# Performance work log

Hardware: AMD Instinct MI355X
Metric: run time of the kernel (lower is better)

Reference implementation:

```python
import jax, jax.numpy as jnp
import numpy as np

N_EMBD = 1024
N_HEAD = 16
HEAD_DIM = N_EMBD // N_HEAD


def setup_inputs() -> dict:
    key = jax.random.key(0)
    ks = jax.random.split(key, 9)
    B, T, C = 2, 2048, N_EMBD
    s = 1.0 / np.sqrt(C)
    inp = {
        "x": jax.random.normal(ks[0], (B, T, C), dtype=jnp.float32),
        "Wq": jax.random.normal(ks[1], (C, C), dtype=jnp.float32) * s,
        "bq": jnp.zeros((C,), dtype=jnp.float32),
        "Wk": jax.random.normal(ks[2], (C, C), dtype=jnp.float32) * s,
        "bk": jnp.zeros((C,), dtype=jnp.float32),
        "Wv": jax.random.normal(ks[3], (C, C), dtype=jnp.float32) * s,
        "bv": jnp.zeros((C,), dtype=jnp.float32),
        "Wo": jax.random.normal(ks[4], (C, C), dtype=jnp.float32) * s,
        "bo": jnp.zeros((C,), dtype=jnp.float32),
    }
    return inp


def reference(x, Wq, bq, Wk, bk, Wv, bv, Wo, bo):
    B, T, C = x.shape
    H, D = N_HEAD, HEAD_DIM
    # projections (torch Linear: x @ W^T + b)
    q = (x @ Wq.T + bq).reshape(B, T, H, D).transpose(0, 2, 1, 3)  # [B,H,T,D]
    k = (x @ Wk.T + bk).reshape(B, T, H, D).transpose(0, 2, 1, 3)
    v = (x @ Wv.T + bv).reshape(B, T, H, D).transpose(0, 2, 1, 3)
    scores = jnp.einsum("bhqd,bhkd->bhqk", q, k) / jnp.sqrt(jnp.asarray(D, x.dtype))
    causal = jnp.tril(jnp.ones((T, T), dtype=bool))
    scores = jnp.where(causal[None, None], scores, jnp.asarray(-jnp.inf, x.dtype))
    weights = jax.nn.softmax(scores, axis=-1)  # [B,H,T,T]
    attended = jnp.einsum("bhqk,bhkd->bhqd", weights, v)
    attended = attended.transpose(0, 2, 1, 3).reshape(B, T, C)
    return attended @ Wo.T + bo
```

## Files before the change

### kernel.cpp

```cpp
#include <hip/hip_runtime.h>

typedef unsigned short u16;
typedef __attribute__((ext_vector_type(8))) __bf16 bf16x8;
typedef __attribute__((ext_vector_type(4))) float f32x4;
typedef __attribute__((ext_vector_type(4))) unsigned int u32x4;

#define MFMA16(a, b, c) __builtin_amdgcn_mfma_f32_16x16x32_bf16(a, b, c, 0, 0, 0)

__device__ __forceinline__ u16 f2bf(float f) {
    unsigned u = __float_as_uint(f);
    u = (u + 0x7FFFu + ((u >> 16) & 1u)) >> 16;
    return (u16)u;
}

__device__ __forceinline__ void gl_lds16(const u16* g, u16* l) {
    __builtin_amdgcn_global_load_lds(
        (const __attribute__((address_space(1))) unsigned int*)g,
        (__attribute__((address_space(3))) unsigned int*)l, 16, 0, 0);
}

static constexpr int Bv = 2, Tv = 2048, Cv = 1024, Hv = 16, Dv = 64;
static constexpr int Mv = Bv * Tv;

static constexpr size_t OFF_XB = 0;
static constexpr size_t OFF_WQ = 4194304;
static constexpr size_t OFF_WK = OFF_WQ + 1048576;
static constexpr size_t OFF_WV = OFF_WK + 1048576;
static constexpr size_t OFF_WO = OFF_WV + 1048576;
static constexpr size_t OFF_Q  = OFF_WO + 1048576;
static constexpr size_t OFF_K  = OFF_Q + 4194304;
static constexpr size_t OFF_VT = OFF_K + 4194304;
static constexpr size_t OFF_A  = OFF_VT + 4194304;

__global__ __launch_bounds__(256) void convert_all(
    const float* __restrict__ x,
    const float* __restrict__ wq, const float* __restrict__ wk,
    const float* __restrict__ wv, const float* __restrict__ wo,
    u16* __restrict__ dst)
{
    int i4 = blockIdx.x * blockDim.x + threadIdx.x;
    if (i4 >= 2097152) return;
    int idx = i4 * 4;
    const float* src; int off;
    if (idx < 4194304) { src = x; off = idx; }
    else {
        int rel = idx - 4194304;
        int j = rel >> 20;
        off = rel & 1048575;
        src = (j == 0) ? wq : (j == 1) ? wk : (j == 2) ? wv : wo;
    }
    float4 v = *(const float4*)(src + off);
    ushort4 o;
    o.x = f2bf(v.x); o.y = f2bf(v.y); o.z = f2bf(v.z); o.w = f2bf(v.w);
    *(ushort4*)(dst + idx) = o;
}

template <bool OUT_BF16, bool ROWBIAS>
__device__ __forceinline__ void gemm128_b64(
    const u16* __restrict__ A, const u16* __restrict__ Wt,
    const float* __restrict__ bias, void* __restrict__ outp,
    int m0, int n0, int N, int K)
{
    __shared__ u16 lA[128 * 64];
    __shared__ u16 lB[128 * 64];
    const int tid  = threadIdx.x;
    const int lane = tid & 63, w = tid >> 6;
    const int quad = lane >> 4, lm = lane & 15;
    const int wm = (w & 1) * 64, wn = (w >> 1) * 64;

    f32x4 zero = {0.f, 0.f, 0.f, 0.f};
    f32x4 acc[4][4];
    #pragma unroll
    for (int mt = 0; mt < 4; mt++)
        #pragma unroll
        for (int nt = 0; nt < 4; nt++) acc[mt][nt] = zero;

    const int rowi = lane >> 3, seg = lane & 7;

    for (int k0 = 0; k0 < K; k0 += 64) {
        #pragma unroll
        for (int i = 0; i < 4; i++) {
            int rbase = w * 32 + i * 8;
            int row = rbase + rowi;
            int gseg = seg ^ (row & 7);
            gl_lds16(A  + (size_t)(m0 + row) * K + k0 + gseg * 8, &lA[rbase * 64]);
            gl_lds16(Wt + (size_t)(n0 + row) * K + k0 + gseg * 8, &lB[rbase * 64]);
        }
        __syncthreads();
        #pragma unroll
        for (int ks = 0; ks < 2; ks++) {
            const int swz = ((ks * 4 + quad) ^ (lm & 7)) * 8;
            bf16x8 af[4], bf[4];
            #pragma unroll
            for (int mt = 0; mt < 4; mt++)
                af[mt] = *(const bf16x8*)&lA[(wm + mt * 16 + lm) * 64 + swz];
            #pragma unroll
            for (int nt = 0; nt < 4; nt++)
                bf[nt] = *(const bf16x8*)&lB[(wn + nt * 16 + lm) * 64 + swz];
            #pragma unroll
            for (int mt = 0; mt < 4; mt++)
                #pragma unroll
                for (int nt = 0; nt < 4; nt++)
                    acc[mt][nt] = MFMA16(af[mt], bf[nt], acc[mt][nt]);
        }
        __syncthreads();
    }

    #pragma unroll
    for (int nt = 0; nt < 4; nt++) {
        int col = n0 + wn + nt * 16 + lm;
        float cb = ROWBIAS ? 0.f : bias[col];
        #pragma unroll
        for (int mt = 0; mt < 4; mt++) {
            #pragma unroll
            for (int r = 0; r < 4; r++) {
                int row = m0 + wm + mt * 16 + quad * 4 + r;
                float v = acc[mt][nt][r] + (ROWBIAS ? bias[row] : cb);
                if (OUT_BF16) ((u16*)outp)[(size_t)row * N + col] = f2bf(v);
                else          ((float*)outp)[(size_t)row * N + col] = v;
            }
        }
    }
}

__global__ __launch_bounds__(256) void gemm_qkv(
    const u16* __restrict__ A,
    const u16* __restrict__ Wq, const u16* __restrict__ Wk, const u16* __restrict__ Wv,
    const float* __restrict__ bq, const float* __restrict__ bk, const float* __restrict__ bv,
    u16* __restrict__ Q, u16* __restrict__ K, u16* __restrict__ VT)
{
    int nb = blockIdx.x;
    int which = nb >> 3;
    if (which == 0) {
        gemm128_b64<true, false>(A, Wq, bq, Q, blockIdx.y * 128, (nb & 7) * 128, Cv, Cv);
    } else if (which == 1) {
        gemm128_b64<true, false>(A, Wk, bk, K, blockIdx.y * 128, (nb & 7) * 128, Cv, Cv);
    } else {
        gemm128_b64<true, true>(Wv, A, bv, VT, (nb & 7) * 128, blockIdx.y * 128, Mv, Cv);
    }
}

__global__ __launch_bounds__(256) void gemm_o64(
    const u16* __restrict__ A, const u16* __restrict__ Wt,
    const float* __restrict__ bias, float* __restrict__ outp)
{
    __shared__ u16 lA[128 * 64];
    __shared__ u16 lB[64 * 64];
    const int tid  = threadIdx.x;
    const int lane = tid & 63, w = tid >> 6;
    const int quad = lane >> 4, lm = lane & 15;
    const int m0 = blockIdx.y * 128, n0 = blockIdx.x * 64;
    const int K = Cv;

    f32x4 zero = {0.f, 0.f, 0.f, 0.f};
    f32x4 acc[2][4];
    #pragma unroll
    for (int mt = 0; mt < 2; mt++)
        #pragma unroll
        for (int nt = 0; nt < 4; nt++) acc[mt][nt] = zero;

    const int rowi = lane >> 3, seg = lane & 7;

    for (int k0 = 0; k0 < K; k0 += 64) {
        #pragma unroll
        for (int i = 0; i < 4; i++) {
            int rbase = w * 32 + i * 8;
            int row = rbase + rowi;
            int gseg = seg ^ (row & 7);
            gl_lds16(A + (size_t)(m0 + row) * K + k0 + gseg * 8, &lA[rbase * 64]);
        }
        {
            int rbase = w * 16, row0 = rbase + rowi, row1 = row0 + 8;
            gl_lds16(Wt + (size_t)(n0 + row0) * K + k0 + (seg ^ (row0 & 7)) * 8, &lB[rbase * 64]);
            gl_lds16(Wt + (size_t)(n0 + row1) * K + k0 + (seg ^ (row1 & 7)) * 8, &lB[(rbase + 8) * 64]);
        }
        __syncthreads();
        #pragma unroll
        for (int ks = 0; ks < 2; ks++) {
            const int swz = ((ks * 4 + quad) ^ (lm & 7)) * 8;
            bf16x8 af[2], bf[4];
            #pragma unroll
            for (int mt = 0; mt < 2; mt++)
                af[mt] = *(const bf16x8*)&lA[(w * 32 + mt * 16 + lm) * 64 + swz];
            #pragma unroll
            for (int nt = 0; nt < 4; nt++)
                bf[nt] = *(const bf16x8*)&lB[(nt * 16 + lm) * 64 + swz];
            #pragma unroll
            for (int mt = 0; mt < 2; mt++)
                #pragma unroll
                for (int nt = 0; nt < 4; nt++)
                    acc[mt][nt] = MFMA16(af[mt], bf[nt], acc[mt][nt]);
        }
        __syncthreads();
    }

    #pragma unroll
    for (int nt = 0; nt < 4; nt++) {
        int col = n0 + nt * 16 + lm;
        float bvv = bias[col];
        #pragma unroll
        for (int mt = 0; mt < 2; mt++) {
            #pragma unroll
            for (int r = 0; r < 4; r++) {
                int row = m0 + w * 32 + mt * 16 + quad * 4 + r;
                outp[(size_t)row * Cv + col] = acc[mt][nt][r] + bvv;
            }
        }
    }
}

__global__ __launch_bounds__(512) void attn(
    const u16* __restrict__ Qp, const u16* __restrict__ Kp,
    const u16* __restrict__ VTg, u16* __restrict__ Op)
{
    __shared__ u16 lK[2][64 * 64];
    __shared__ u16 lVT[2][64 * 64];
    __shared__ u16 lP[8][32][72];

    const int tid  = threadIdx.x;
    const int lane = tid & 63, w = tid >> 6;
    const int g = w >> 2, wl = w & 3;
    const int quad = lane >> 4, lm = lane & 15;

    const int idx  = blockIdx.x;
    const int half = idx >> 8;
    const int grp  = idx & 255;
    const int bh   = (half << 4) | (grp >> 4);
    const int j    = grp & 15;
    const int qt   = half ? j : 15 - j;
    const int h = bh & 15, b = bh >> 4;

    const int qb = qt * 128;
    const size_t headoff = (size_t)b * Tv * Cv + (size_t)h * Dv;
    const size_t vthead  = (size_t)h * 64 * Mv + (size_t)b * Tv;

    bf16x8 qf[2][2];
    #pragma unroll
    for (int nt = 0; nt < 2; nt++) {
        const u16* qptr = Qp + headoff + (size_t)(qb + wl * 32 + nt * 16 + lm) * Cv + quad * 8;
        qf[0][nt] = *(const bf16x8*)(qptr);
        qf[1][nt] = *(const bf16x8*)(qptr + 32);
    }

    f32x4 zero = {0.f, 0.f, 0.f, 0.f};
    f32x4 oacc[2][4];
    #pragma unroll
    for (int mt = 0; mt < 2; mt++)
        #pragma unroll
        for (int nt = 0; nt < 4; nt++) oacc[mt][nt] = zero;
    float Lp[2] = {0.f, 0.f};

    const float SC = 0.18033688011112042f;
    const int rowi = lane >> 3, seg = lane & 7;

    auto stage = [&](int kt) {
        const int k0 = kt * 64;
        #pragma unroll
        for (int hf = 0; hf < 2; hf++) {
            int rbase = wl * 16 + hf * 8;
            int row = rbase + rowi;
            int gseg = seg ^ (row & 7);
            gl_lds16(Kp + headoff + (size_t)(k0 + row) * Cv + gseg * 8, &lK[g][rbase * 64]);
            gl_lds16(VTg + vthead + (size_t)row * Mv + k0 + gseg * 8, &lVT[g][rbase * 64]);
        }
    };

    auto body = [&](int kt, bool domask) __attribute__((always_inline)) {
        const int k0 = kt * 64;
        f32x4 stt[4][2];
        #pragma unroll
        for (int mt = 0; mt < 4; mt++)
            #pragma unroll
            for (int nt = 0; nt < 2; nt++) stt[mt][nt] = zero;
        #pragma unroll
        for (int ks = 0; ks < 2; ks++) {
            #pragma unroll
            for (int mt = 0; mt < 4; mt++) {
                bf16x8 kf = *(const bf16x8*)
                    &lK[g][(mt * 16 + lm) * 64 + (((ks * 4 + quad) ^ (lm & 7)) * 8)];
                #pragma unroll
                for (int nt = 0; nt < 2; nt++)
                    stt[mt][nt] = MFMA16(kf, qf[ks][nt], stt[mt][nt]);
            }
        }
        #pragma unroll
        for (int mt = 0; mt < 4; mt++) {
            #pragma unroll
            for (int nt = 0; nt < 2; nt++) {
                const int keyb = k0 + mt * 16 + quad * 4;
                const int qrow = qb + wl * 32 + nt * 16 + lm;
                float e0 = __builtin_amdgcn_exp2f(fmaf(stt[mt][nt][0], SC, -16.f));
                float e1 = __builtin_amdgcn_exp2f(fmaf(stt[mt][nt][1], SC, -16.f));
                float e2 = __builtin_amdgcn_exp2f(fmaf(stt[mt][nt][2], SC, -16.f));
                float e3 = __builtin_amdgcn_exp2f(fmaf(stt[mt][nt][3], SC, -16.f));
                if (domask) {
                    if (keyb + 0 > qrow) e0 = 0.f;
                    if (keyb + 1 > qrow) e1 = 0.f;
                    if (keyb + 2 > qrow) e2 = 0.f;
                    if (keyb + 3 > qrow) e3 = 0.f;
                }
                Lp[nt] += e0 + e1 + e2 + e3;
                ushort4 pk;
                pk.x = (u16)(__float_as_uint(e0) >> 16);
                pk.y = (u16)(__float_as_uint(e1) >> 16);
                pk.z = (u16)(__float_as_uint(e2) >> 16);
                pk.w = (u16)(__float_as_uint(e3) >> 16);
                *(ushort4*)&lP[w][nt * 16 + lm][mt * 16 + quad * 4] = pk;
            }
        }
        #pragma unroll
        for (int ks = 0; ks < 2; ks++) {
            bf16x8 pf[2];
            #pragma unroll
            for (int mt = 0; mt < 2; mt++)
                pf[mt] = *(const bf16x8*)&lP[w][mt * 16 + lm][ks * 32 + quad * 8];
            #pragma unroll
            for (int nt = 0; nt < 4; nt++) {
                bf16x8 vf = *(const bf16x8*)
                    &lVT[g][(nt * 16 + lm) * 64 + (((ks * 4 + quad) ^ (lm & 7)) * 8)];
                #pragma unroll
                for (int mt = 0; mt < 2; mt++)
                    oacc[mt][nt] = MFMA16(pf[mt], vf, oacc[mt][nt]);
            }
        }
    };

    for (int i = 0; i < qt; i++) {
        if (i) __syncthreads();
        stage(2 * i + g);
        __syncthreads();
        body(2 * i + g, false);
    }
    if (qt) __syncthreads();
    stage(2 * qt + g);
    __syncthreads();
    body(2 * qt + g, true);
    __syncthreads();

    float* lO = (float*)&lP[0][0][0];
    float* lL = lO + 32 * 256;
    const int t = tid & 255;
    if (g == 1) {
        #pragma unroll
        for (int mt = 0; mt < 2; mt++)
            #pragma unroll
            for (int nt = 0; nt < 4; nt++)
                #pragma unroll
                for (int r = 0; r < 4; r++)
                    lO[(mt * 16 + nt * 4 + r) * 256 + t] = oacc[mt][nt][r];
        lL[t] = Lp[0];
        lL[256 + t] = Lp[1];
    }
    __syncthreads();
    if (g == 0) {
        #pragma unroll
        for (int mt = 0; mt < 2; mt++)
            #pragma unroll
            for (int nt = 0; nt < 4; nt++)
                #pragma unroll
                for (int r = 0; r < 4; r++)
                    oacc[mt][nt][r] += lO[(mt * 16 + nt * 4 + r) * 256 + t];
        Lp[0] += lL[t];
        Lp[1] += lL[256 + t];

        float Lred[2];
        #pragma unroll
        for (int nt = 0; nt < 2; nt++) {
            float L = Lp[nt];
            L += __shfl_xor(L, 16, 64);
            L += __shfl_xor(L, 32, 64);
            Lred[nt] = 1.0f / L;
        }
        #pragma unroll
        for (int mt = 0; mt < 2; mt++) {
            float inv[4];
            #pragma unroll
            for (int r = 0; r < 4; r++)
                inv[r] = __shfl(Lred[mt], (lane & 48) | (quad * 4 + r), 64);
            #pragma unroll
            for (int nt = 0; nt < 4; nt++) {
                #pragma unroll
                for (int r = 0; r < 4; r++) {
                    int row = qb + wl * 32 + mt * 16 + quad * 4 + r;
                    Op[headoff + (size_t)row * Cv + nt * 16 + lm] = f2bf(oacc[mt][nt][r] * inv[r]);
                }
            }
        }
    }
}

extern "C" void kernel_launch(void* const* d_in, const int* in_sizes, int n_in,
                              void* d_out, int out_size, void* d_ws, size_t ws_size,
                              hipStream_t stream) {
    const float* x  = (const float*)d_in[0];
    const float* Wq = (const float*)d_in[1];
    const float* bq = (const float*)d_in[2];
    const float* Wk = (const float*)d_in[3];
    const float* bk = (const float*)d_in[4];
    const float* Wv = (const float*)d_in[5];
    const float* bv = (const float*)d_in[6];
    const float* Wo = (const float*)d_in[7];
    const float* bo = (const float*)d_in[8];
    u16* ws = (u16*)d_ws;

    convert_all<<<8192, 256, 0, stream>>>(x, Wq, Wk, Wv, Wo, ws);

    gemm_qkv<<<dim3(24, 32), 256, 0, stream>>>(
        ws + OFF_XB, ws + OFF_WQ, ws + OFF_WK, ws + OFF_WV,
        bq, bk, bv, ws + OFF_Q, ws + OFF_K, ws + OFF_VT);

    attn<<<512, 512, 0, stream>>>(ws + OFF_Q, ws + OFF_K, ws + OFF_VT, ws + OFF_A);

    gemm_o64<<<dim3(16, 32), 256, 0, stream>>>(ws + OFF_A, ws + OFF_WO, bo, (float*)d_out);
}
```

Before: 184.1 us.

## Double-buffer LDS tiles in projection GEMMs and swizzle block order across XCDs

Both projection GEMMs now use two LDS buffers, so the async global-to-LDS load of the next K tile is issued before computing on the current one, with one barrier per step instead of two. The grids are flattened to 1D and remapped so consecutive blocks on the same XCD (bid&7 round-robin) cover neighbouring output tiles, meant to improve L2 reuse of the A and weight rows. The cost is doubled LDS per block (64KB in gemm_qkv), which may lower occupancy.

New measurement: 182.3 us. No clear change (-0.9%).

```diff
diff --git a/kernel.cpp b/kernel.cpp
--- a/kernel.cpp
+++ b/kernel.cpp
@@ -57,16 +57,17 @@
 
 template <bool OUT_BF16, bool ROWBIAS>
 __device__ __forceinline__ void gemm128_b64(
+    u16* __restrict__ lA0, u16* __restrict__ lB0,
+    u16* __restrict__ lA1, u16* __restrict__ lB1,
     const u16* __restrict__ A, const u16* __restrict__ Wt,
     const float* __restrict__ bias, void* __restrict__ outp,
     int m0, int n0, int N, int K)
 {
-    __shared__ u16 lA[128 * 64];
-    __shared__ u16 lB[128 * 64];
     const int tid  = threadIdx.x;
     const int lane = tid & 63, w = tid >> 6;
     const int quad = lane >> 4, lm = lane & 15;
     const int wm = (w & 1) * 64, wn = (w >> 1) * 64;
+    const int rowi = lane >> 3, seg = lane & 7;
 
     f32x4 zero = {0.f, 0.f, 0.f, 0.f};
     f32x4 acc[4][4];
@@ -75,35 +76,47 @@
         #pragma unroll
         for (int nt = 0; nt < 4; nt++) acc[mt][nt] = zero;
 
-    const int rowi = lane >> 3, seg = lane & 7;
-
-    for (int k0 = 0; k0 < K; k0 += 64) {
+    auto stage = [&](u16* dA, u16* dB, int k0) __attribute__((always_inline)) {
         #pragma unroll
         for (int i = 0; i < 4; i++) {
             int rbase = w * 32 + i * 8;
             int row = rbase + rowi;
             int gseg = seg ^ (row & 7);
-            gl_lds16(A  + (size_t)(m0 + row) * K + k0 + gseg * 8, &lA[rbase * 64]);
-            gl_lds16(Wt + (size_t)(n0 + row) * K + k0 + gseg * 8, &lB[rbase * 64]);
-        }
-        __syncthreads();
+            gl_lds16(A  + (size_t)(m0 + row) * K + k0 + gseg * 8, &dA[rbase * 64]);
+            gl_lds16(Wt + (size_t)(n0 + row) * K + k0 + gseg * 8, &dB[rbase * 64]);
+        }
+    };
+    auto compute = [&](const u16* sA, const u16* sB) __attribute__((always_inline)) {
         #pragma unroll
         for (int ks = 0; ks < 2; ks++) {
             const int swz = ((ks * 4 + quad) ^ (lm & 7)) * 8;
             bf16x8 af[4], bf[4];
             #pragma unroll
             for (int mt = 0; mt < 4; mt++)
-                af[mt] = *(const bf16x8*)&lA[(wm + mt * 16 + lm) * 64 + swz];
+                af[mt] = *(const bf16x8*)&sA[(wm + mt * 16 + lm) * 64 + swz];
             #pragma unroll
             for (int nt = 0; nt < 4; nt++)
-                bf[nt] = *(const bf16x8*)&lB[(wn + nt * 16 + lm) * 64 + swz];
+                bf[nt] = *(const bf16x8*)&sB[(wn + nt * 16 + lm) * 64 + swz];
             #pragma unroll
             for (int mt = 0; mt < 4; mt++)
                 #pragma unroll
                 for (int nt = 0; nt < 4; nt++)
                     acc[mt][nt] = MFMA16(af[mt], bf[nt], acc[mt][nt]);
         }
+    };
+
+    const int NT = K >> 6;
+    stage(lA0, lB0, 0);
+    __syncthreads();
+    for (int t = 0; t < NT; t += 2) {
+        if (t + 1 < NT) stage(lA1, lB1, (t + 1) << 6);
+        compute(lA0, lB0);
         __syncthreads();
+        if (t + 2 < NT) stage(lA0, lB0, (t + 2) << 6);
+        if (t + 1 < NT) {
+            compute(lA1, lB1);
+            __syncthreads();
+        }
     }
 
     #pragma unroll
@@ -129,14 +142,23 @@
     const float* __restrict__ bq, const float* __restrict__ bk, const float* __restrict__ bv,
     u16* __restrict__ Q, u16* __restrict__ K, u16* __restrict__ VT)
 {
-    int nb = blockIdx.x;
-    int which = nb >> 3;
+    __shared__ u16 lA0[128 * 64];
+    __shared__ u16 lB0[128 * 64];
+    __shared__ u16 lA1[128 * 64];
+    __shared__ u16 lB1[128 * 64];
+
+    int bid = blockIdx.x;
+    int sw  = (bid & 7) * 96 + (bid >> 3);
+    int g2  = sw >> 5;
+    int row = sw & 31;
+    int which = g2 >> 3, col = g2 & 7;
+
     if (which == 0) {
-        gemm128_b64<true, false>(A, Wq, bq, Q, blockIdx.y * 128, (nb & 7) * 128, Cv, Cv);
+        gemm128_b64<true, false>(lA0, lB0, lA1, lB1, A, Wq, bq, Q, row * 128, col * 128, Cv, Cv);
     } else if (which == 1) {
-        gemm128_b64<true, false>(A, Wk, bk, K, blockIdx.y * 128, (nb & 7) * 128, Cv, Cv);
+        gemm128_b64<true, false>(lA0, lB0, lA1, lB1, A, Wk, bk, K, row * 128, col * 128, Cv, Cv);
     } else {
-        gemm128_b64<true, true>(Wv, A, bv, VT, (nb & 7) * 128, blockIdx.y * 128, Mv, Cv);
+        gemm128_b64<true, true>(lA0, lB0, lA1, lB1, Wv, A, bv, VT, col * 128, row * 128, Mv, Cv);
     }
 }
 
@@ -144,13 +166,21 @@
     const u16* __restrict__ A, const u16* __restrict__ Wt,
     const float* __restrict__ bias, float* __restrict__ outp)
 {
-    __shared__ u16 lA[128 * 64];
-    __shared__ u16 lB[64 * 64];
+    __shared__ u16 lA0[128 * 64];
+    __shared__ u16 lA1[128 * 64];
+    __shared__ u16 lB0[64 * 64];
+    __shared__ u16 lB1[64 * 64];
+
     const int tid  = threadIdx.x;
     const int lane = tid & 63, w = tid >> 6;
     const int quad = lane >> 4, lm = lane & 15;
-    const int m0 = blockIdx.y * 128, n0 = blockIdx.x * 64;
+
+    int bid = blockIdx.x;
+    int sw  = (bid & 7) * 64 + (bid >> 3);
+    const int n0 = (sw >> 5) * 64;
+    const int m0 = (sw & 31) * 128;
     const int K = Cv;
+    const int rowi = lane >> 3, seg = lane & 7;
 
     f32x4 zero = {0.f, 0.f, 0.f, 0.f};
     f32x4 acc[2][4];
@@ -159,39 +189,51 @@
         #pragma unroll
         for (int nt = 0; nt < 4; nt++) acc[mt][nt] = zero;
 
-    const int rowi = lane >> 3, seg = lane & 7;
-
-    for (int k0 = 0; k0 < K; k0 += 64) {
+    auto stage = [&](u16* dA, u16* dB, int k0) __attribute__((always_inline)) {
         #pragma unroll
         for (int i = 0; i < 4; i++) {
             int rbase = w * 32 + i * 8;
             int row = rbase + rowi;
             int gseg = seg ^ (row & 7);
-            gl_lds16(A + (size_t)(m0 + row) * K + k0 + gseg * 8, &lA[rbase * 64]);
+            gl_lds16(A + (size_t)(m0 + row) * K + k0 + gseg * 8, &dA[rbase * 64]);
         }
         {
             int rbase = w * 16, row0 = rbase + rowi, row1 = row0 + 8;
-            gl_lds16(Wt + (size_t)(n0 + row0) * K + k0 + (seg ^ (row0 & 7)) * 8, &lB[rbase * 64]);
-            gl_lds16(Wt + (size_t)(n0 + row1) * K + k0 + (seg ^ (row1 & 7)) * 8, &lB[(rbase + 8) * 64]);
-        }
-        __syncthreads();
+            gl_lds16(Wt + (size_t)(n0 + row0) * K + k0 + (seg ^ (row0 & 7)) * 8, &dB[rbase * 64]);
+            gl_lds16(Wt + (size_t)(n0 + row1) * K + k0 + (seg ^ (row1 & 7)) * 8, &dB[(rbase + 8) * 64]);
+        }
+    };
+    auto compute = [&](const u16* sA, const u16* sB) __attribute__((always_inline)) {
         #pragma unroll
         for (int ks = 0; ks < 2; ks++) {
             const int swz = ((ks * 4 + quad) ^ (lm & 7)) * 8;
             bf16x8 af[2], bf[4];
             #pragma unroll
             for (int mt = 0; mt < 2; mt++)
-                af[mt] = *(const bf16x8*)&lA[(w * 32 + mt * 16 + lm) * 64 + swz];
+                af[mt] = *(const bf16x8*)&sA[(w * 32 + mt * 16 + lm) * 64 + swz];
             #pragma unroll
             for (int nt = 0; nt < 4; nt++)
-                bf[nt] = *(const bf16x8*)&lB[(nt * 16 + lm) * 64 + swz];
+                bf[nt] = *(const bf16x8*)&sB[(nt * 16 + lm) * 64 + swz];
             #pragma unroll
             for (int mt = 0; mt < 2; mt++)
                 #pragma unroll
                 for (int nt = 0; nt < 4; nt++)
                     acc[mt][nt] = MFMA16(af[mt], bf[nt], acc[mt][nt]);
         }
+    };
+
+    const int NT = K >> 6;
+    stage(lA0, lB0, 0);
+    __syncthreads();
+    for (int t = 0; t < NT; t += 2) {
+        if (t + 1 < NT) stage(lA1, lB1, (t + 1) << 6);
+        compute(lA0, lB0);
         __syncthreads();
+        if (t + 2 < NT) stage(lA0, lB0, (t + 2) << 6);
+        if (t + 1 < NT) {
+            compute(lA1, lB1);
+            __syncthreads();
+        }
     }
 
     #pragma unroll
@@ -405,11 +447,11 @@
 
     convert_all<<<8192, 256, 0, stream>>>(x, Wq, Wk, Wv, Wo, ws);
 
-    gemm_qkv<<<dim3(24, 32), 256, 0, stream>>>(
+    gemm_qkv<<<768, 256, 0, stream>>>(
         ws + OFF_XB, ws + OFF_WQ, ws + OFF_WK, ws + OFF_WV,
         bq, bk, bv, ws + OFF_Q, ws + OFF_K, ws + OFF_VT);
 
     attn<<<512, 512, 0, stream>>>(ws + OFF_Q, ws + OFF_K, ws + OFF_VT, ws + OFF_A);
 
-    gemm_o64<<<dim3(16, 32), 256, 0, stream>>>(ws + OFF_A, ws + OFF_WO, bo, (float*)d_out);
-}
+    gemm_o64<<<512, 256, 0, stream>>>(ws + OFF_A, ws + OFF_WO, bo, (float*)d_out);
+}
```
